# Performance work log

Hardware: AMD Instinct MI355X
Metric: run time of the kernel (lower is better)

Reference implementation:

```python
import jax, jax.numpy as jnp
import numpy as np

THETA = 10000.0

def apply_rope(x, positions):
    # x: [B, H, S, D_head], positions: [S] int
    d = x.shape[-1]
    inv_freq = THETA ** (-jnp.arange(0, d, 2, dtype=jnp.float32) / d)  # [d/2]
    ang = positions.astype(jnp.float32)[:, None] * inv_freq[None, :]   # [S, d/2]
    cos, sin = jnp.cos(ang), jnp.sin(ang)                              # broadcast over B,H
    x1, x2 = x[..., 0::2], x[..., 1::2]
    r1 = x1 * cos - x2 * sin
    r2 = x1 * sin + x2 * cos
    return jnp.stack([r1, r2], axis=-1).reshape(x.shape)


def setup_inputs() -> dict:
    key = jax.random.key(0)
    ks = jax.random.split(key, 5)
    B, S, D = 4, 2048, 1024
    scale = 1.0 / np.sqrt(D)
    return {
        "x": jax.random.normal(ks[0], (B, S, D), dtype=jnp.float32),
        "Wq": jax.random.normal(ks[1], (D, D), dtype=jnp.float32) * scale,
        "Wk": jax.random.normal(ks[2], (D, D), dtype=jnp.float32) * scale,
        "Wv": jax.random.normal(ks[3], (D, D), dtype=jnp.float32) * scale,
        "Wo": jax.random.normal(ks[4], (D, D), dtype=jnp.float32) * scale,
        "token_positions": jnp.arange(S, dtype=jnp.int32),
    }


def reference(x, Wq, Wk, Wv, Wo, token_positions):
    B, S, D = x.shape
    H = 16
    hd = D // H
    # fused QKV projection (weights stored [out, in], y = x @ W^T, no bias)
    qkv_w = jnp.concatenate([Wq, Wk, Wv], axis=0)          # [3D, D]
    qkv = x @ qkv_w.T                                      # [B, S, 3D]
    q, k, v = jnp.split(qkv, 3, axis=-1)
    # [B, S, D] -> [B, H, S, hd]
    def split_heads(t):
        return t.reshape(B, S, H, hd).transpose(0, 2, 1, 3)
    q, k, v = split_heads(q), split_heads(k), split_heads(v)
    q = apply_rope(q, token_positions)
    k = apply_rope(k, token_positions)
    scores = jnp.einsum('bhqd,bhkd->bhqk', q, k) / jnp.sqrt(jnp.float32(hd))
    causal = jnp.tril(jnp.ones((S, S), dtype=bool))        # True = attend
    scores = jnp.where(causal[None, None], scores, -jnp.inf)
    attn = jax.nn.softmax(scores, axis=-1)
    out = jnp.einsum('bhqk,bhkd->bhqd', attn, v)           # [B, H, S, hd]
    out = out.transpose(0, 2, 1, 3).reshape(B, S, D)
    return out @ Wo.T
```

## Files before the change

kernel.cpp:

```cpp
#include <hip/hip_runtime.h>
#include <hip/hip_bf16.h>


typedef __bf16 bf16x8 __attribute__((ext_vector_type(8)));
typedef float f32x4 __attribute__((ext_vector_type(4)));
typedef unsigned short u16x8 __attribute__((ext_vector_type(8)));

#define DEV static __device__ __forceinline__

DEV unsigned short f2bf(float f) {
  unsigned int u = __builtin_bit_cast(unsigned int, f);
  u += 0x7FFFu + ((u >> 16) & 1u);
  return (unsigned short)(u >> 16);
}
DEV float bf2f(unsigned short h) {
  unsigned int u = ((unsigned int)h) << 16;
  return __builtin_bit_cast(float, u);
}
DEV bf16x8 ld_bf8(const unsigned short* p) {
  union { u16x8 u; bf16x8 b; } c;
  c.u = *reinterpret_cast<const u16x8*>(p);
  return c.b;
}
DEV unsigned int pk2(float a, float b) {
  unsigned int r;
  asm("v_cvt_pk_bf16_f32 %0, %1, %2" : "=v"(r) : "v"(a), "v"(b));
  return r;
}

DEV void gload_lds16(const unsigned short* src, unsigned short* dst) {
  __builtin_amdgcn_global_load_lds(
      (const __attribute__((address_space(1))) void*)src,
      (__attribute__((address_space(3))) void*)dst, 16, 0, 0);
}

DEV void stage_tile(const unsigned short* g, int ldg, unsigned short* lds,
                    int wave, int lane) {
  int rl = lane >> 3;
  int c16 = lane & 7;
#pragma unroll
  for (int i = 0; i < 4; ++i) {
    int row = i * 32 + wave * 8 + rl;
    int sc16 = c16 ^ (row & 7);
    const unsigned short* src = g + (size_t)row * ldg + sc16 * 8;
    unsigned short* dst = lds + (i * 32 + wave * 8) * 64;
    gload_lds16(src, dst);
  }
}

DEV bf16x8 lds_frag(const unsigned short* lds, int row, int c16) {
  return ld_bf8(lds + row * 64 + ((c16 ^ (row & 7)) << 3));
}

__global__ void k_f32_to_bf16(const float* __restrict__ in,
                              unsigned short* __restrict__ out, int n4) {
  int i = blockIdx.x * blockDim.x + threadIdx.x;
  if (i < n4) {
    float4 v = reinterpret_cast<const float4*>(in)[i];
    uint2 o;
    o.x = pk2(v.x, v.y);
    o.y = pk2(v.z, v.w);
    reinterpret_cast<uint2*>(out)[i] = o;
  }
}

__global__ void k_conv_w(const float* __restrict__ Wq, const float* __restrict__ Wk,
                         const float* __restrict__ Wv, const float* __restrict__ Wo,
                         unsigned short* __restrict__ Wb, unsigned short* __restrict__ Wob) {
  int i = blockIdx.x * blockDim.x + threadIdx.x;
  int which = i >> 18, j = i & 262143;
  const float* src = (which == 0) ? Wq : (which == 1) ? Wk : (which == 2) ? Wv : Wo;
  unsigned short* dst = (which == 3) ? Wob : Wb + (size_t)which * 1048576;
  float4 v = reinterpret_cast<const float4*>(src)[j];
  uint2 o;
  o.x = pk2(v.x, v.y);
  o.y = pk2(v.z, v.w);
  reinterpret_cast<uint2*>(dst)[j] = o;
}

__global__ void k_rope_table(const int* __restrict__ pos, float* __restrict__ tab) {
  int idx = blockIdx.x * blockDim.x + threadIdx.x;
  if (idx >= 2048 * 32) return;
  int s = idx >> 5, i = idx & 31;
  double inv = pow(10000.0, -(double)(2 * i) / 64.0);
  double ang = (double)pos[s] * inv;
  tab[idx * 2]     = (float)cos(ang);
  tab[idx * 2 + 1] = (float)sin(ang);
}

__global__ __launch_bounds__(256) void k_gemm_qkv(
    const unsigned short* __restrict__ A, const unsigned short* __restrict__ W,
    unsigned short* __restrict__ Qh, unsigned short* __restrict__ Kh,
    unsigned short* __restrict__ Vt, const float* __restrict__ tab) {
  const int Kd = 1024, S = 2048;
  __shared__ __align__(16) unsigned short SM[128 * 132];
  unsigned short* As = SM;
  unsigned short* Bs = SM + 8192;
  int m0 = blockIdx.x * 128, n0 = blockIdx.y * 128;
  int wave = threadIdx.x >> 6, lane = threadIdx.x & 63;
  int wm = wave >> 1, wn = wave & 1;
  int lr = lane & 15, lk = lane >> 4;
  const unsigned short* Ag = A + (size_t)m0 * Kd;
  const unsigned short* Wg = W + (size_t)n0 * Kd;
  f32x4 acc[4][4] = {};
  for (int k0 = 0; k0 < Kd; k0 += 64) {
    stage_tile(Ag + k0, Kd, As, wave, lane);
    stage_tile(Wg + k0, Kd, Bs, wave, lane);
    __syncthreads();
#pragma unroll
    for (int ks = 0; ks < 2; ++ks) {
      bf16x8 a[4], b[4];
#pragma unroll
      for (int fm = 0; fm < 4; ++fm) a[fm] = lds_frag(As, wm * 64 + fm * 16 + lr, ks * 4 + lk);
#pragma unroll
      for (int fn = 0; fn < 4; ++fn) b[fn] = lds_frag(Bs, wn * 64 + fn * 16 + lr, ks * 4 + lk);
#pragma unroll
      for (int fm = 0; fm < 4; ++fm)
#pragma unroll
        for (int fn = 0; fn < 4; ++fn)
          acc[fm][fn] = __builtin_amdgcn_mfma_f32_16x16x32_bf16(a[fm], b[fn], acc[fm][fn], 0, 0, 0);
    }
    __syncthreads();
  }

  int t = n0 >> 10;
  int b = m0 >> 11, s_base = m0 & 2047;
  if (t == 2) {
#pragma unroll
    for (int fm = 0; fm < 4; ++fm) {
      int r0 = wm * 64 + fm * 16 + lk * 4;
#pragma unroll
      for (int fn = 0; fn < 4; ++fn) {
        int c = wn * 64 + fn * 16 + lr;
        uint2 w;
        w.x = pk2(acc[fm][fn][0], acc[fm][fn][1]);
        w.y = pk2(acc[fm][fn][2], acc[fm][fn][3]);
        *reinterpret_cast<uint2*>(SM + c * 132 + r0) = w;
      }
    }
    __syncthreads();
    int h0 = (n0 - 2048) >> 6;
#pragma unroll
    for (int it = 0; it < 16; ++it) {
      int idx = it * 256 + threadIdx.x;
      int c = idx >> 5, ch = idx & 31;
      int h = h0 + (c >> 6), d = c & 63;
      uint2 w = *reinterpret_cast<const uint2*>(SM + c * 132 + ch * 4);
      *reinterpret_cast<uint2*>(Vt + (((size_t)(b * 16 + h) * 64) + d) * S + s_base + ch * 4) = w;
    }
  } else {
    unsigned short* dst0 = (t == 0) ? Qh : Kh;
    int h0 = (n0 & 1023) >> 6;
#pragma unroll
    for (int fm = 0; fm < 4; ++fm) {
      int r0 = wm * 64 + fm * 16 + lk * 4;
#pragma unroll
      for (int fn = 0; fn < 4; ++fn) {
        int c = wn * 64 + fn * 16 + lr;
        int d = c & 63;
        int ri = d >> 1;
        bool odd = d & 1;
#pragma unroll
        for (int r = 0; r < 4; ++r) {
          int s = s_base + r0 + r;
          float2 cs = reinterpret_cast<const float2*>(tab)[s * 32 + ri];
          float v = acc[fm][fn][r];
          float other = __shfl_xor(v, 1);
          float res = odd ? (other * cs.y + v * cs.x)
                          : (v * cs.x - other * cs.y);
          SM[(r0 + r) * 132 + c] = f2bf(res);
        }
      }
    }
    __syncthreads();
#pragma unroll
    for (int it = 0; it < 16; ++it) {
      int idx = it * 256 + threadIdx.x;
      int sloc = idx >> 5;
      int c = (idx & 31) * 4;
      int h = h0 + (c >> 6), d = c & 63;
      uint2 w = *reinterpret_cast<const uint2*>(SM + sloc * 132 + c);
      *reinterpret_cast<uint2*>(dst0 + (((size_t)(b * 16 + h)) * S + s_base + sloc) * 64 + d) = w;
    }
  }
}

__global__ __launch_bounds__(512) void k_attn(
    const unsigned short* __restrict__ Qh, const unsigned short* __restrict__ Kh,
    const unsigned short* __restrict__ Vt, unsigned short* __restrict__ Obuf) {
  const int S = 2048;
  const float KF = 0.18033688f;
  const float NEGH = -34.624667f;
  int bh = blockIdx.x;
  int b = bh >> 4, h = bh & 15;
  int wave = threadIdx.x >> 6, lane = threadIdx.x & 63;
  int lr = lane & 15, lk = lane >> 4;
  int yy = (int)gridDim.y - 1 - (int)blockIdx.y;
  int qt = 2 * yy + (wave >> 2);
  int q0 = qt * 128 + (wave & 3) * 32;
  const unsigned short* Qp = Qh + (size_t)bh * S * 64;
  const unsigned short* Kp = Kh + (size_t)bh * S * 64;
  const unsigned short* Vp = Vt + (size_t)bh * 64 * S;

  __shared__ __align__(16) unsigned short Ks[2][64 * 64];
  __shared__ __align__(16) unsigned short Vs[2][64 * 64];
  __shared__ __align__(16) unsigned short P_all[8][32][64];
  char* pw = (char*)&P_all[wave][0][0];

  auto STAGE = [&](int buf, int kv0) {
    int rl = lane >> 3, c16 = lane & 7;
    int row = wave * 8 + rl;
    int sc = (c16 ^ rl) << 3;
    gload_lds16(Kp + (size_t)(kv0 + row) * 64 + sc, &Ks[buf][wave * 8 * 64]);
    gload_lds16(Vp + (size_t)row * S + kv0 + sc,    &Vs[buf][wave * 8 * 64]);
  };

  bf16x8 qb[2][2];
#pragma unroll
  for (int mi = 0; mi < 2; ++mi)
#pragma unroll
    for (int ks = 0; ks < 2; ++ks)
      qb[mi][ks] = ld_bf8(Qp + (size_t)(q0 + mi * 16 + lr) * 64 + ks * 32 + lk * 8);

  f32x4 acc_o[4][2] = {};
  float l_run[2] = {0.f, 0.f};
  int my_nt = (q0 + 31) / 64 + 1;
  int NT = 2 * (2 * yy + 1) + 2;

  STAGE(0, 0);
  __syncthreads();

  for (int t = 0; t < NT; ++t) {
    int cur = t & 1;
    if (t + 1 < NT) STAGE(cur ^ 1, (t + 1) * 64);
    if (t < my_nt) {
      int kv0 = t * 64;
      bf16x8 ka[4][2];
#pragma unroll
      for (int ni = 0; ni < 4; ++ni)
#pragma unroll
        for (int ks = 0; ks < 2; ++ks)
          ka[ni][ks] = lds_frag(&Ks[cur][0], ni * 16 + lr, ks * 4 + lk);
      f32x4 st[4][2] = {};
      __builtin_amdgcn_s_setprio(1);
#pragma unroll
      for (int ni = 0; ni < 4; ++ni)
#pragma unroll
        for (int mi = 0; mi < 2; ++mi) {
          st[ni][mi] = __builtin_amdgcn_mfma_f32_16x16x32_bf16(ka[ni][0], qb[mi][0], st[ni][mi], 0, 0, 0);
          st[ni][mi] = __builtin_amdgcn_mfma_f32_16x16x32_bf16(ka[ni][1], qb[mi][1], st[ni][mi], 0, 0, 0);
        }
      __builtin_amdgcn_s_setprio(0);
      bf16x8 va[4][2];
#pragma unroll
      for (int nf = 0; nf < 4; ++nf)
#pragma unroll
        for (int ks = 0; ks < 2; ++ks)
          va[nf][ks] = lds_frag(&Vs[cur][0], nf * 16 + lr, ks * 4 + lk);

      if (kv0 + 63 > q0) {
#pragma unroll
        for (int mi = 0; mi < 2; ++mi) {
          int row = q0 + mi * 16 + lr;
#pragma unroll
          for (int ni = 0; ni < 4; ++ni)
#pragma unroll
            for (int r = 0; r < 4; ++r)
              if (kv0 + ni * 16 + lk * 4 + r > row) st[ni][mi][r] = -3e38f;
        }
      }
#pragma unroll
      for (int mi = 0; mi < 2; ++mi) {
        int prow = mi * 16 + lr;
        char* rowp = pw + prow * 128;
        int swz = (lr & 7) << 4;
        float rs = 0.f;
#pragma unroll
        for (int ni = 0; ni < 4; ++ni) {
          float p0 = __builtin_amdgcn_exp2f(fmaf(st[ni][mi][0], KF, NEGH));
          float p1 = __builtin_amdgcn_exp2f(fmaf(st[ni][mi][1], KF, NEGH));
          float p2 = __builtin_amdgcn_exp2f(fmaf(st[ni][mi][2], KF, NEGH));
          float p3 = __builtin_amdgcn_exp2f(fmaf(st[ni][mi][3], KF, NEGH));
          rs += (p0 + p1) + (p2 + p3);
          uint2 w; w.x = pk2(p0, p1); w.y = pk2(p2, p3);
          *reinterpret_cast<uint2*>(rowp + ((ni * 32 + lk * 8) ^ swz)) = w;
        }
        rs += __shfl_xor(rs, 16);
        rs += __shfl_xor(rs, 32);
        l_run[mi] += rs;
      }
      bf16x8 pb[2][2];
#pragma unroll
      for (int mi = 0; mi < 2; ++mi) {
        int prow = mi * 16 + lr;
        int swz = (lr & 7) << 4;
#pragma unroll
        for (int ks = 0; ks < 2; ++ks)
          pb[mi][ks] = ld_bf8((const unsigned short*)(pw + prow * 128 + ((ks * 64 + lk * 16) ^ swz)));
      }
      __builtin_amdgcn_s_setprio(1);
#pragma unroll
      for (int nf = 0; nf < 4; ++nf)
#pragma unroll
        for (int mi = 0; mi < 2; ++mi) {
          acc_o[nf][mi] = __builtin_amdgcn_mfma_f32_16x16x32_bf16(va[nf][0], pb[mi][0], acc_o[nf][mi], 0, 0, 0);
          acc_o[nf][mi] = __builtin_amdgcn_mfma_f32_16x16x32_bf16(va[nf][1], pb[mi][1], acc_o[nf][mi], 0, 0, 0);
        }
      __builtin_amdgcn_s_setprio(0);
    }
    __syncthreads();
  }

#pragma unroll
  for (int mi = 0; mi < 2; ++mi) {
    float inv_l = 1.f / l_run[mi];
    int q = q0 + mi * 16 + lr;
    size_t base = ((size_t)b * S + q) * 1024 + h * 64;
#pragma unroll
    for (int nf = 0; nf < 4; ++nf) {
      uint2 w;
      w.x = pk2(acc_o[nf][mi][0] * inv_l, acc_o[nf][mi][1] * inv_l);
      w.y = pk2(acc_o[nf][mi][2] * inv_l, acc_o[nf][mi][3] * inv_l);
      *reinterpret_cast<uint2*>(Obuf + base + nf * 16 + lk * 4) = w;
    }
  }
}

__global__ __launch_bounds__(256) void k_gemm_out(
    const unsigned short* __restrict__ A, const unsigned short* __restrict__ W,
    float* __restrict__ C) {
  const int Kd = 1024;
  __shared__ __align__(16) unsigned short As[128 * 64];
  __shared__ __align__(16) unsigned short Bs[128 * 64];
  int m0 = blockIdx.x * 128, n0 = blockIdx.y * 128;
  int wave = threadIdx.x >> 6, lane = threadIdx.x & 63;
  int wm = wave >> 1, wn = wave & 1;
  int lr = lane & 15, lk = lane >> 4;
  const unsigned short* Ag = A + (size_t)m0 * Kd;
  const unsigned short* Wg = W + (size_t)n0 * Kd;
  f32x4 acc[4][4] = {};
  for (int k0 = 0; k0 < Kd; k0 += 64) {
    stage_tile(Ag + k0, Kd, As, wave, lane);
    stage_tile(Wg + k0, Kd, Bs, wave, lane);
    __syncthreads();
#pragma unroll
    for (int ks = 0; ks < 2; ++ks) {
      bf16x8 a[4], b[4];
#pragma unroll
      for (int fm = 0; fm < 4; ++fm) a[fm] = lds_frag(As, wm * 64 + fm * 16 + lr, ks * 4 + lk);
#pragma unroll
      for (int fn = 0; fn < 4; ++fn) b[fn] = lds_frag(Bs, wn * 64 + fn * 16 + lr, ks * 4 + lk);
#pragma unroll
      for (int fm = 0; fm < 4; ++fm)
#pragma unroll
        for (int fn = 0; fn < 4; ++fn)
          acc[fm][fn] = __builtin_amdgcn_mfma_f32_16x16x32_bf16(a[fm], b[fn], acc[fm][fn], 0, 0, 0);
    }
    __syncthreads();
  }
#pragma unroll
  for (int fm = 0; fm < 4; ++fm)
#pragma unroll
    for (int fn = 0; fn < 4; ++fn)
#pragma unroll
      for (int r = 0; r < 4; ++r)
        C[(size_t)(m0 + wm * 64 + fm * 16 + lk * 4 + r) * 1024 + n0 + wn * 64 + fn * 16 + lr] =
            acc[fm][fn][r];
}

extern "C" void kernel_launch(void* const* d_in, const int* in_sizes, int n_in,
                              void* d_out, int out_size, void* d_ws, size_t ws_size,
                              hipStream_t stream) {
  const float* x  = (const float*)d_in[0];
  const float* Wq = (const float*)d_in[1];
  const float* Wk = (const float*)d_in[2];
  const float* Wv = (const float*)d_in[3];
  const float* Wo = (const float*)d_in[4];
  const int* pos  = (const int*)d_in[5];
  float* out = (float*)d_out;
  char* ws = (char*)d_ws;

  unsigned short* xb  = (unsigned short*)(ws);
  unsigned short* Wb  = (unsigned short*)(ws + 16777216);
  unsigned short* Wob = (unsigned short*)(ws + 23068672);
  unsigned short* Qh  = (unsigned short*)(ws + 25165824);
  unsigned short* Kh  = (unsigned short*)(ws + 41943040);
  unsigned short* Ob  = (unsigned short*)(ws + 58720256);
  unsigned short* Vt  = (unsigned short*)(ws + 75497472);
  float* tab          = (float*)(ws + 92274688);
  (void)in_sizes; (void)n_in; (void)out_size; (void)ws_size;

  k_f32_to_bf16<<<8192, 256, 0, stream>>>(x, xb, 2097152);
  k_conv_w<<<4096, 256, 0, stream>>>(Wq, Wk, Wv, Wo, Wb, Wob);
  k_rope_table<<<256, 256, 0, stream>>>(pos, tab);

  dim3 g1(64, 24);
  k_gemm_qkv<<<g1, 256, 0, stream>>>(xb, Wb, Qh, Kh, Vt, tab);
  dim3 ga(64, 8);
  k_attn<<<ga, 512, 0, stream>>>(Qh, Kh, Vt, Ob);
  dim3 g2(64, 8);
  k_gemm_out<<<g2, 256, 0, stream>>>(Ob, Wob, out);
}
```

Baseline: 177.8 us.

## Split RoPE out of QKV GEMM epilogue and remap blocks per XCD

Removes the RoPE rotation from the QKV GEMM epilogue and moves it into a separate elementwise kernel that rewrites Q and K in place using the cos/sin table. The GEMM now uses a 1D grid whose block IDs are remapped so consecutive tiles land on the same XCD, aiming at better L2 reuse. The Q/K epilogue now writes scalar bf16 values directly to global memory instead of staging through LDS with vectorized stores. This adds an extra launch and an extra read/write pass over Q and K, and the scattered 2-byte stores may coalesce worse.

```diff
diff --git a/kernel.cpp b/kernel.cpp
--- a/kernel.cpp
+++ b/kernel.cpp
@@ -88,15 +88,44 @@
   tab[idx * 2 + 1] = (float)sin(ang);
 }
 
+__global__ __launch_bounds__(256) void k_rope(unsigned short* __restrict__ Qh,
+                                              unsigned short* __restrict__ Kh,
+                                              const float* __restrict__ tab) {
+  int idx = blockIdx.x * blockDim.x + threadIdx.x;
+  int which = idx >> 20;
+  int j = idx & 1048575;
+  int db = (j & 7) * 8;
+  int s = (j >> 3) & 2047;
+  unsigned short* buf = which ? Kh : Qh;
+  unsigned short* p = buf + (size_t)j * 8;
+  uint4 v = *reinterpret_cast<const uint4*>(p);
+  const float4* tp = reinterpret_cast<const float4*>(tab + s * 64 + db);
+  float4 t0 = tp[0], t1 = tp[1];
+  unsigned int r[4];
+  float cs[4][2] = {{t0.x, t0.y}, {t0.z, t0.w}, {t1.x, t1.y}, {t1.z, t1.w}};
+  unsigned int vv[4] = {v.x, v.y, v.z, v.w};
+#pragma unroll
+  for (int pq = 0; pq < 4; ++pq) {
+    float x1 = bf2f((unsigned short)(vv[pq] & 0xFFFF));
+    float x2 = bf2f((unsigned short)(vv[pq] >> 16));
+    r[pq] = pk2(x1 * cs[pq][0] - x2 * cs[pq][1], x1 * cs[pq][1] + x2 * cs[pq][0]);
+  }
+  *reinterpret_cast<uint4*>(p) = make_uint4(r[0], r[1], r[2], r[3]);
+}
+
 __global__ __launch_bounds__(256) void k_gemm_qkv(
     const unsigned short* __restrict__ A, const unsigned short* __restrict__ W,
     unsigned short* __restrict__ Qh, unsigned short* __restrict__ Kh,
-    unsigned short* __restrict__ Vt, const float* __restrict__ tab) {
+    unsigned short* __restrict__ Vt) {
   const int Kd = 1024, S = 2048;
   __shared__ __align__(16) unsigned short SM[128 * 132];
   unsigned short* As = SM;
   unsigned short* Bs = SM + 8192;
-  int m0 = blockIdx.x * 128, n0 = blockIdx.y * 128;
+  int id = blockIdx.x;
+  int xcd = id & 7, pos = id >> 3;
+  int nid = xcd * 192 + pos;
+  int nIdx = nid % 24, mIdx = nid / 24;
+  int m0 = mIdx * 128, n0 = nIdx * 128;
   int wave = threadIdx.x >> 6, lane = threadIdx.x & 63;
   int wm = wave >> 1, wn = wave & 1;
   int lr = lane & 15, lk = lane >> 4;
@@ -123,7 +152,7 @@
     __syncthreads();
   }
 
-  int t = n0 >> 10;
+  int t = nIdx >> 3;
   int b = m0 >> 11, s_base = m0 & 2047;
   if (t == 2) {
 #pragma unroll
@@ -139,48 +168,31 @@
       }
     }
     __syncthreads();
-    int h0 = (n0 - 2048) >> 6;
+    int h0 = (nIdx - 16) * 2;
 #pragma unroll
     for (int it = 0; it < 16; ++it) {
-      int idx = it * 256 + threadIdx.x;
-      int c = idx >> 5, ch = idx & 31;
+      int idx2 = it * 256 + threadIdx.x;
+      int c = idx2 >> 5, ch = idx2 & 31;
       int h = h0 + (c >> 6), d = c & 63;
       uint2 w = *reinterpret_cast<const uint2*>(SM + c * 132 + ch * 4);
       *reinterpret_cast<uint2*>(Vt + (((size_t)(b * 16 + h) * 64) + d) * S + s_base + ch * 4) = w;
     }
   } else {
     unsigned short* dst0 = (t == 0) ? Qh : Kh;
-    int h0 = (n0 & 1023) >> 6;
+    int h0 = (nIdx & 7) * 2;
 #pragma unroll
     for (int fm = 0; fm < 4; ++fm) {
       int r0 = wm * 64 + fm * 16 + lk * 4;
 #pragma unroll
       for (int fn = 0; fn < 4; ++fn) {
         int c = wn * 64 + fn * 16 + lr;
-        int d = c & 63;
-        int ri = d >> 1;
-        bool odd = d & 1;
+        int h = h0 + (c >> 6), d = c & 63;
 #pragma unroll
         for (int r = 0; r < 4; ++r) {
           int s = s_base + r0 + r;
-          float2 cs = reinterpret_cast<const float2*>(tab)[s * 32 + ri];
-          float v = acc[fm][fn][r];
-          float other = __shfl_xor(v, 1);
-          float res = odd ? (other * cs.y + v * cs.x)
-                          : (v * cs.x - other * cs.y);
-          SM[(r0 + r) * 132 + c] = f2bf(res);
+          dst0[(((size_t)(b * 16 + h)) * S + s) * 64 + d] = f2bf(acc[fm][fn][r]);
         }
       }
-    }
-    __syncthreads();
-#pragma unroll
-    for (int it = 0; it < 16; ++it) {
-      int idx = it * 256 + threadIdx.x;
-      int sloc = idx >> 5;
-      int c = (idx & 31) * 4;
-      int h = h0 + (c >> 6), d = c & 63;
-      uint2 w = *reinterpret_cast<const uint2*>(SM + sloc * 132 + c);
-      *reinterpret_cast<uint2*>(dst0 + (((size_t)(b * 16 + h)) * S + s_base + sloc) * 64 + d) = w;
     }
   }
 }
@@ -394,8 +406,8 @@
   k_conv_w<<<4096, 256, 0, stream>>>(Wq, Wk, Wv, Wo, Wb, Wob);
   k_rope_table<<<256, 256, 0, stream>>>(pos, tab);
 
-  dim3 g1(64, 24);
-  k_gemm_qkv<<<g1, 256, 0, stream>>>(xb, Wb, Qh, Kh, Vt, tab);
+  k_gemm_qkv<<<1536, 256, 0, stream>>>(xb, Wb, Qh, Kh, Vt);
+  k_rope<<<8192, 256, 0, stream>>>(Qh, Kh, tab);
   dim3 ga(64, 8);
   k_attn<<<ga, 512, 0, stream>>>(Qh, Kh, Vt, Ob);
   dim3 g2(64, 8);
```

Result: slower. 183.5 us (+3.2%).
